# Kernel tuning notes

Measured on AMD Instinct MI355X. Metric: run time of the kernel, lower is better.

## Reference

```python
import jax, jax.numpy as jnp
import numpy as np

B, D, E, K, HID, RH, NL, EMB = 4096, 1024, 8, 2, 512, 256, 24, 32


def _ln(y, g, b, eps=1e-5):
    mu = y.mean(-1, keepdims=True)
    var = y.var(-1, keepdims=True)
    return (y - mu) / jnp.sqrt(var + eps) * g + b


def setup_inputs() -> dict:
    key = jax.random.key(0)
    ks = jax.random.split(key, 16)
    s = 0.02
    return {
        "h": jax.random.normal(ks[0], (B, D), jnp.float32),
        "x": jax.random.normal(ks[1], (B, D), jnp.float32),
        "layer_idx": 5,
        "layer_emb": jax.random.normal(ks[2], (NL, EMB)) * s,
        "phase_emb": jax.random.normal(ks[3], (2, EMB)) * s,
        "Wr1": jax.random.normal(ks[4], (2 * D + 2 * EMB, RH)) * s,
        "br1": jnp.zeros((RH,)),
        "lnr_g": jnp.ones((RH,)),
        "lnr_b": jnp.zeros((RH,)),
        "Wr2": jax.random.normal(ks[5], (RH, E)) * s,
        "br2": jnp.zeros((E,)),
        "W1": jax.random.normal(ks[6], (E, 2 * D, HID)) * s,
        "b1": jnp.zeros((E, HID)),
        "ln1_g": jnp.ones((E, HID)),
        "ln1_b": jnp.zeros((E, HID)),
        "W2": jax.random.normal(ks[7], (E, HID, 4 * D)) * s,
        "b2": jnp.zeros((E, 4 * D)),
        "Wa": jax.random.normal(ks[8], (E, D, D)) * s,
        "ba": jnp.zeros((E, D)),
        "Wb": jax.random.normal(ks[9], (E, D, D)) * s,
        "bb": jnp.zeros((E, D)),
        "Wg": jax.random.normal(ks[10], (E, D, D)) * s,
        "bg": jnp.zeros((E, D)),
        "Wv": jax.random.normal(ks[11], (E, D, D)) * s,
        "bv": jnp.zeros((E, D)),
    }


def reference(h, x, layer_idx, layer_emb, phase_emb, Wr1, br1, lnr_g, lnr_b,
              Wr2, br2, W1, b1, ln1_g, ln1_b, W2, b2,
              Wa, ba, Wb, bb, Wg, bg, Wv, bv):
    Bn = h.shape[0]
    # --- router ---
    le = jnp.broadcast_to(layer_emb[layer_idx], (Bn, EMB))
    pe = jnp.broadcast_to(phase_emb[0], (Bn, EMB))  # phase='equilibrium' -> idx 0
    ri = jnp.concatenate([h, x, le, pe], axis=-1)   # [B, 2D+64]
    rhid = jax.nn.gelu(_ln(ri @ Wr1 + br1, lnr_g, lnr_b), approximate=False)
    logits = rhid @ Wr2 + br2                       # [B, E]
    top_vals, top_idx = jax.lax.top_k(logits, K)    # [B, K]
    w = jax.nn.softmax(top_vals, axis=-1)           # [B, K]
    # --- all experts (vectorized over E), then gather top-k per token ---
    hx = jnp.concatenate([h, x], axis=-1)           # [B, 2D]
    hid = jnp.einsum('bi,eio->ebo', hx, W1) + b1[:, None]          # [E, B, HID]
    hid = jax.nn.gelu(_ln(hid, ln1_g[:, None], ln1_b[:, None]), approximate=False)
    feats = jnp.einsum('ebh,eho->ebo', hid, W2) + b2[:, None]      # [E, B, 4D]
    af, bf, gf, vf = jnp.split(feats, 4, axis=-1)
    alpha = jax.nn.sigmoid(jnp.einsum('ebd,edo->ebo', af, Wa) + ba[:, None])
    beta = jax.nn.softplus(jnp.einsum('ebd,edo->ebo', bf, Wb) + bb[:, None])
    gate = jax.nn.sigmoid(jnp.einsum('ebd,edo->ebo', gf, Wg) + bg[:, None])
    vcd = jnp.einsum('ebd,edo->ebo', vf, Wv) + bv[:, None]
    allo = jnp.stack([alpha, beta, gate, vcd])       # [4, E, B, D]
    sel = allo[:, top_idx, jnp.arange(Bn)[:, None]]  # [4, B, K, D]
    out = jnp.einsum('bk,obkd->obd', w, sel)         # [4, B, D]
    return out
```

## Files before the change

kernel.cpp:

```cpp
#include <hip/hip_runtime.h>
#include <hip/hip_bf16.h>

#define B_TOK   4096
#define D_DIM   1024
#define E_NUM   8
#define HID_DIM 512
#define RH_DIM  256
#define EMB_DIM 32
#define NPAIR   (B_TOK * 2)
#define CPAD    32

typedef __attribute__((ext_vector_type(8))) short    bf16x8;
typedef __attribute__((ext_vector_type(8))) unsigned short u16x8;
typedef __attribute__((ext_vector_type(4))) unsigned short u16x4;
typedef __attribute__((ext_vector_type(4))) float    f32x4;

__device__ __forceinline__ unsigned short f2bf(float f) {
    union { float f; unsigned u; } v; v.f = f;
    unsigned r = (v.u + 0x7fffu + ((v.u >> 16) & 1u)) >> 16;
    return (unsigned short)r;
}
__device__ __forceinline__ float bf2f(unsigned short b) {
    union { unsigned u; float f; } v; v.u = ((unsigned)b) << 16;
    return v.f;
}

__device__ __forceinline__ void glds16(const void* g, void* l) {
    __builtin_amdgcn_global_load_lds(
        (const __attribute__((address_space(1))) unsigned int*)g,
        (__attribute__((address_space(3))) unsigned int*)l, 16, 0, 0);
}

__device__ inline float apply_act(float v, int a) {
    if (a == 0 || a == 2) return 1.f / (1.f + __expf(-v));
    if (a == 1) return fmaxf(v, 0.f) + __logf(1.f + __expf(-fabsf(v)));
    return v;
}

__global__ void k_hxbf(const float* __restrict__ h, const float* __restrict__ x,
                       unsigned short* __restrict__ hi, unsigned short* __restrict__ lo) {
    int gid = blockIdx.x * 256 + threadIdx.x;
    int token = gid >> 8;
    int c0 = (gid & 255) * 8;
    const float* src = (c0 < 1024) ? (h + (size_t)token * 1024 + c0)
                                   : (x + (size_t)token * 1024 + c0 - 1024);
    u16x8 oh, ol;
#pragma unroll
    for (int j = 0; j < 8; ++j) {
        float f = src[j];
        unsigned short hb = f2bf(f);
        oh[j] = hb;
        ol[j] = f2bf(f - bf2f(hb));
    }
    size_t o = (size_t)gid * 8;
    *(u16x8*)(hi + o) = oh;
    *(u16x8*)(lo + o) = ol;
}

__global__ void k_cvtflat(const float* __restrict__ in, unsigned short* __restrict__ o8) {
    size_t gid = (size_t)blockIdx.x * 256 + threadIdx.x;
    const float4* s = (const float4*)(in + gid * 8);
    float4 a = s[0], b = s[1];
    u16x8 v;
    v[0] = f2bf(a.x); v[1] = f2bf(a.y); v[2] = f2bf(a.z); v[3] = f2bf(a.w);
    v[4] = f2bf(b.x); v[5] = f2bf(b.y); v[6] = f2bf(b.z); v[7] = f2bf(b.w);
    *(u16x8*)(o8 + gid * 8) = v;
}

template<bool SPLIT>
__global__ void k_convW(const float* __restrict__ in0, const float* __restrict__ in1,
                        const float* __restrict__ in2, const float* __restrict__ in3,
                        unsigned short* __restrict__ oh, unsigned short* __restrict__ ol,
                        int K, int N, int eper) {
    int z = blockIdx.z;
    int e = z % eper, m = z / eper;
    const float* in = (m == 0 ? in0 : m == 1 ? in1 : m == 2 ? in2 : in3) + (size_t)e * K * N;
    int n  = blockIdx.x * 256 + threadIdx.x;
    int kg = blockIdx.y;
    const float* ip = in + (size_t)kg * 8 * N + n;
    u16x8 hv, lv;
#pragma unroll
    for (int j = 0; j < 8; ++j) {
        float f = ip[(size_t)j * N];
        unsigned short hb = f2bf(f);
        hv[j] = hb;
        if (SPLIT) lv[j] = f2bf(f - bf2f(hb));
    }
    size_t o = (size_t)z * K * N + ((size_t)kg * N + n) * 8;
    *(u16x8*)(oh + o) = hv;
    if (SPLIT) *(u16x8*)(ol + o) = lv;
}

__global__ void k_bfuse(const float* __restrict__ b2,
                        const float* __restrict__ bo0, const float* __restrict__ bo1,
                        const float* __restrict__ bo2, const float* __restrict__ bo3,
                        const unsigned short* __restrict__ wsc,
                        float* __restrict__ bfused) {
    int zp = blockIdx.y; int e = zp & 7, o = zp >> 3;
    int col = blockIdx.x * 256 + threadIdx.x;
    __shared__ float b2s[1024];
    for (int i = threadIdx.x; i < 1024; i += 256)
        b2s[i] = b2[(size_t)e * 4096 + o * 1024 + i];
    __syncthreads();
    const unsigned short* W = wsc + (size_t)zp * 1024 * 1024;
    float acc = 0.f;
    for (int dg = 0; dg < 128; ++dg) {
        u16x8 w = *(const u16x8*)&W[((size_t)dg * 1024 + col) * 8];
#pragma unroll
        for (int j = 0; j < 8; ++j) acc += b2s[dg * 8 + j] * bf2f(w[j]);
    }
    const float* bo = (o == 0) ? bo0 : (o == 1) ? bo1 : (o == 2) ? bo2 : bo3;
    bfused[(size_t)e * 4096 + o * 1024 + col] = acc + bo[(size_t)e * 1024 + col];
}

__global__ void k_route(const float* __restrict__ Pf,
                        const int* __restrict__ lidx,
                        const float* __restrict__ layer_emb,
                        const float* __restrict__ phase_emb,
                        const float* __restrict__ Wr1, const float* __restrict__ br1,
                        const float* __restrict__ lnr_g, const float* __restrict__ lnr_b,
                        const float* __restrict__ Wr2, const float* __restrict__ br2,
                        float* __restrict__ pair_w,
                        int* __restrict__ lists, int* __restrict__ counts) {
    int b = blockIdx.x, t = threadIdx.x;
    __shared__ float sv[RH_DIM];
    __shared__ float a1[4], a2[4], mv[2];
    __shared__ float wsum[4][E_NUM];
    __shared__ float lg[E_NUM];
    __shared__ int sei[2];

    float rc = br1[t];
    {
        int li = lidx[0];
        for (int k = 0; k < EMB_DIM; ++k)
            rc += layer_emb[li * EMB_DIM + k] * Wr1[(2048 + k) * RH_DIM + t];
        for (int k = 0; k < EMB_DIM; ++k)
            rc += phase_emb[k] * Wr1[(2080 + k) * RH_DIM + t];
    }

    size_t idx = (size_t)b * RH_DIM + t;
    const size_t kstride = (size_t)B_TOK * RH_DIM;
    float y = ((Pf[idx] + Pf[idx + kstride]) + (Pf[idx + 2 * kstride] + Pf[idx + 3 * kstride]))
              + rc;
    float s1 = y, s2 = y * y;
    for (int o = 32; o; o >>= 1) { s1 += __shfl_down(s1, o); s2 += __shfl_down(s2, o); }
    if ((t & 63) == 0) { a1[t >> 6] = s1; a2[t >> 6] = s2; }
    __syncthreads();
    if (t == 0) {
        float S1 = a1[0] + a1[1] + a1[2] + a1[3];
        float S2 = a2[0] + a2[1] + a2[2] + a2[3];
        float mu = S1 / 256.f;
        mv[0] = mu;
        mv[1] = rsqrtf(S2 / 256.f - mu * mu + 1e-5f);
    }
    __syncthreads();
    float n = (y - mv[0]) * mv[1] * lnr_g[t] + lnr_b[t];
    sv[t] = 0.5f * n * (1.f + erff(n * 0.70710678118654752f));
    __syncthreads();

    {
        int e = t & 7, c = t >> 3;
        float part = 0.f;
#pragma unroll
        for (int jj = 0; jj < 8; ++jj)
            part += sv[c * 8 + jj] * Wr2[(c * 8 + jj) * E_NUM + e];
        part += __shfl_down(part, 8);
        part += __shfl_down(part, 16);
        part += __shfl_down(part, 32);
        if ((t & 63) < 8) wsum[t >> 6][e] = part;
    }
    __syncthreads();
    if (t < E_NUM)
        lg[t] = br2[t] + wsum[0][t] + wsum[1][t] + wsum[2][t] + wsum[3][t];
    __syncthreads();
    if (t == 0) {
        float v0 = -1e30f; int i0 = 0;
        for (int e = 0; e < E_NUM; ++e) if (lg[e] > v0) { v0 = lg[e]; i0 = e; }
        float v1 = -1e30f; int i1 = 0;
        for (int e = 0; e < E_NUM; ++e) if (e != i0 && lg[e] > v1) { v1 = lg[e]; i1 = e; }
        float e1 = expf(v1 - v0);
        pair_w[2 * b] = 1.f / (1.f + e1);
        pair_w[2 * b + 1] = e1 / (1.f + e1);
        sei[0] = i0; sei[1] = i1;
    }
    __syncthreads();
    if (t < 2) {
        int e = sei[t];
        int pos = atomicAdd(&counts[e * CPAD], 1);
        lists[e * B_TOK + pos] = 2 * b + t;
    }
}

__global__ void k_meta(const int* __restrict__ counts, const int* __restrict__ lists,
                       int* __restrict__ rowmap, int* __restrict__ row_e,
                       int* __restrict__ qof) {
    int q = blockIdx.x * 256 + threadIdx.x;
    int off_[E_NUM + 1]; off_[0] = 0;
#pragma unroll
    for (int i = 0; i < E_NUM; ++i) off_[i + 1] = off_[i] + counts[i * CPAD];
    int e = 0;
    while (e < E_NUM - 1 && q >= off_[e + 1]) ++e;
    int p = lists[e * B_TOK + (q - off_[e])];
    rowmap[q] = p;
    row_e[q] = e;
    qof[p] = q;
}

__global__ void k_lngelu(const float* __restrict__ hidp, const float* __restrict__ b1,
                         unsigned short* __restrict__ hidb, const int* __restrict__ row_e,
                         const float* __restrict__ g, const float* __restrict__ bb) {
    int q = blockIdx.x, t = threadIdx.x;
    int e = row_e[q];
    const size_t st = (size_t)NPAIR * HID_DIM;
    size_t o0 = (size_t)q * HID_DIM + t;
    float y0 = hidp[o0] + hidp[o0 + st] + b1[e * HID_DIM + t];
    float y1 = hidp[o0 + 256] + hidp[o0 + 256 + st] + b1[e * HID_DIM + t + 256];
    float s1 = y0 + y1, s2 = y0 * y0 + y1 * y1;
    for (int o = 32; o; o >>= 1) { s1 += __shfl_down(s1, o); s2 += __shfl_down(s2, o); }
    __shared__ float a1[4], a2[4], mv[2];
    if ((t & 63) == 0) { a1[t >> 6] = s1; a2[t >> 6] = s2; }
    __syncthreads();
    if (t == 0) {
        float S1 = a1[0] + a1[1] + a1[2] + a1[3];
        float S2 = a2[0] + a2[1] + a2[2] + a2[3];
        float mu = S1 / 512.f;
        mv[0] = mu;
        mv[1] = rsqrtf(S2 / 512.f - mu * mu + 1e-5f);
    }
    __syncthreads();
    const float* ge = g + e * HID_DIM;
    const float* be = bb + e * HID_DIM;
    float mu = mv[0], ir = mv[1];
    float n0 = (y0 - mu) * ir * ge[t] + be[t];
    float n1 = (y1 - mu) * ir * ge[t + 256] + be[t + 256];
    unsigned short* orow = hidb + (size_t)q * HID_DIM;
    orow[t]       = f2bf(0.5f * n0 * (1.f + erff(n0 * 0.70710678118654752f)));
    orow[t + 256] = f2bf(0.5f * n1 * (1.f + erff(n1 * 0.70710678118654752f)));
}

__global__ void k_comb(const unsigned short* __restrict__ sel,
                       const int* __restrict__ qof, const float* __restrict__ pw,
                       float* __restrict__ out) {
    int b = blockIdx.x, o = blockIdx.y;
    int c = threadIdx.x * 4;
    int q0 = qof[2 * b], q1 = qof[2 * b + 1];
    float w0 = pw[2 * b], w1 = pw[2 * b + 1];
    u16x4 a = __builtin_nontemporal_load((const u16x4*)(sel + (size_t)q0 * 4096 + o * 1024 + c));
    u16x4 bq = __builtin_nontemporal_load((const u16x4*)(sel + (size_t)q1 * 4096 + o * 1024 + c));
    f32x4 r;
#pragma unroll
    for (int j = 0; j < 4; ++j)
        r[j] = w0 * apply_act(bf2f(a[j]), o) + w1 * apply_act(bf2f(bq[j]), o);
    __builtin_nontemporal_store(r, (f32x4*)(out + ((size_t)o * B_TOK + b) * D_DIM + c));
}

template<int MODE, bool SPLIT, bool AGATHER, bool ZPIN>
__global__ __launch_bounds__(256)
void k_mm(const unsigned short* __restrict__ A, const unsigned short* __restrict__ Alo,
          int lda, int rowshift, int acol0,
          const unsigned short* __restrict__ Wp, const unsigned short* __restrict__ Wlo,
          size_t wstride,
          const float* __restrict__ bias, int bstride,
          float* __restrict__ Cf, unsigned short* __restrict__ Cb, int ldc,
          const int* __restrict__ counts, const int* __restrict__ rowmap, int Mfix,
          int N, int Kdim, int nz_e,
          float* __restrict__ outp, const float* __restrict__ pw) {
    const int gx = gridDim.x, gy = gridDim.y;
    unsigned fb = blockIdx.x + gx * (blockIdx.y + gy * blockIdx.z);
    int bx, byy, bz;
    if (ZPIN) {
        const unsigned nmn = gx * gy;
        unsigned xcd = fb & 7u, s = fb >> 3;
        bz  = xcd + 8u * (s / nmn);
        unsigned inner = s % nmn;
        bx  = inner % gx;
        byy = inner / gx;
    } else {
        unsigned xcd = fb & 7u, sb = fb >> 3;
        unsigned G = xcd + 8u * (sb / gx);
        bx  = sb % gx;
        byy = G % gy;
        bz  = G / gy;
    }

    const int e  = bz % nz_e;
    const int zq = bz / nz_e;
    int cnt = Mfix, base = 0;
    if (counts) {
        cnt = 0;
#pragma unroll
        for (int i = 0; i < E_NUM; ++i) {
            int c = counts[i * CPAD];
            if (i < e) base += c;
            if (i == e) cnt = c;
        }
    }
    const int m0 = byy * 128;
    if (m0 >= cnt) return;
    const int n0 = bx * 128;

    const size_t woff = (MODE == 8) ? (size_t)bz * wstride
                      : (MODE == 1 || MODE == 9) ? (size_t)e * wstride
                      : (size_t)e * wstride + (size_t)zq * Kdim * N;
    const unsigned short* W  = Wp + woff;
    const unsigned short* Wl = SPLIT ? (Wlo + woff) : nullptr;
    const float* bptr = (MODE == 1 || MODE == 9) ? bias + (size_t)e * bstride : nullptr;
    const int acol = acol0 + zq * Kdim;

    constexpr int ABUF = SPLIT ? 8192 : 4096;
    __shared__ unsigned short Alds[2][ABUF];
    __shared__ unsigned short Blds[2][ABUF];

    const int tid  = threadIdx.x;
    const int lane = tid & 63;
    const int wid  = tid >> 6;
    const int c0 = tid, c1 = tid + 256;
    const int r0 = c0 >> 2, r1 = c1 >> 2;

    auto aoff_of = [&](int r, int cq) -> size_t {
        int rr = m0 + r; if (rr >= cnt) rr = cnt - 1;
        int qg = base + rr;
        int row = AGATHER ? (rowmap[qg] >> rowshift)
                          : (MODE == 8 ? e * 512 + qg : qg);
        int slot = cq ^ ((r >> 1) & 3);
        return (size_t)row * lda + acol + (slot << 3);
    };
    size_t aoff0 = aoff_of(r0, c0 & 3);
    size_t aoff1 = aoff_of(r1, c1 & 3);
    const unsigned short* a0 = A + aoff0;
    const unsigned short* a1 = A + aoff1;
    const unsigned short* al0 = SPLIT ? Alo + aoff0 : nullptr;
    const unsigned short* al1 = SPLIT ? Alo + aoff1 : nullptr;
    size_t boff0 = ((size_t)(c0 >> 7) * N + n0 + (c0 & 127)) * 8;
    size_t boff1 = ((size_t)(c1 >> 7) * N + n0 + (c1 & 127)) * 8;
    const unsigned short* b0 = W + boff0;
    const unsigned short* b1 = W + boff1;
    const unsigned short* bl0 = SPLIT ? Wl + boff0 : nullptr;
    const unsigned short* bl1 = SPLIT ? Wl + boff1 : nullptr;

    const int d0 = c0 * 8, d1 = c1 * 8;
    const size_t bstep = (size_t)32 * N;

    auto stage = [&](int buf) {
        glds16(a0, &Alds[buf][d0]);
        glds16(a1, &Alds[buf][d1]);
        glds16(b0, &Blds[buf][d0]);
        glds16(b1, &Blds[buf][d1]);
        if constexpr (SPLIT) {
            glds16(al0, &Alds[buf][4096 + d0]);
            glds16(al1, &Alds[buf][4096 + d1]);
            glds16(bl0, &Blds[buf][4096 + d0]);
            glds16(bl1, &Blds[buf][4096 + d1]);
            al0 += 32; al1 += 32; bl0 += bstep; bl1 += bstep;
        }
        a0 += 32; a1 += 32; b0 += bstep; b1 += bstep;
    };

    const int wm = wid >> 1, wn = wid & 1;
    const int lr = lane & 15, lg = lane >> 4;
    const int aslot = (lg ^ ((lr >> 1) & 3)) << 3;

    f32x4 acc[4][4];
#pragma unroll
    for (int i = 0; i < 4; ++i)
#pragma unroll
        for (int j = 0; j < 4; ++j) acc[i][j] = (f32x4){0.f, 0.f, 0.f, 0.f};

    auto compute = [&](int b) {
        bf16x8 af[4], bfr[4];
#pragma unroll
        for (int i = 0; i < 4; ++i)
            af[i] = *(const bf16x8*)&Alds[b][(wm * 64 + i * 16 + lr) * 32 + aslot];
#pragma unroll
        for (int i = 0; i < 4; ++i)
            bfr[i] = *(const bf16x8*)&Blds[b][((lg << 7) + wn * 64 + i * 16 + lr) * 8];
        __builtin_amdgcn_s_setprio(1);
#pragma unroll
        for (int mi = 0; mi < 4; ++mi)
#pragma unroll
            for (int ni = 0; ni < 4; ++ni)
                acc[mi][ni] = __builtin_amdgcn_mfma_f32_16x16x32_bf16(af[mi], bfr[ni], acc[mi][ni], 0, 0, 0);
        if constexpr (SPLIT) {
            bf16x8 afl[4], bfl[4];
#pragma unroll
            for (int i = 0; i < 4; ++i)
                afl[i] = *(const bf16x8*)&Alds[b][4096 + (wm * 64 + i * 16 + lr) * 32 + aslot];
#pragma unroll
            for (int i = 0; i < 4; ++i)
                bfl[i] = *(const bf16x8*)&Blds[b][4096 + ((lg << 7) + wn * 64 + i * 16 + lr) * 8];
#pragma unroll
            for (int mi = 0; mi < 4; ++mi)
#pragma unroll
                for (int ni = 0; ni < 4; ++ni) {
                    acc[mi][ni] = __builtin_amdgcn_mfma_f32_16x16x32_bf16(af[mi],  bfl[ni], acc[mi][ni], 0, 0, 0);
                    acc[mi][ni] = __builtin_amdgcn_mfma_f32_16x16x32_bf16(afl[mi], bfr[ni], acc[mi][ni], 0, 0, 0);
                }
        }
        __builtin_amdgcn_s_setprio(0);
        __builtin_amdgcn_sched_barrier(0);
    };

    const int niter = Kdim / 32;
    stage(0);
    asm volatile("s_waitcnt vmcnt(0)" ::: "memory");
    __builtin_amdgcn_s_barrier();
    __builtin_amdgcn_sched_barrier(0);
    int cur = 0;
    for (int it = 0; it < niter; ++it) {
        const bool more = (it + 1 < niter);
        if (more) stage(cur ^ 1);
        compute(cur);
        if (more) {
            asm volatile("s_waitcnt vmcnt(0)" ::: "memory");
            __builtin_amdgcn_s_barrier();
            __builtin_amdgcn_sched_barrier(0);
        }
        cur ^= 1;
    }

    float bv[4];
#pragma unroll
    for (int ni = 0; ni < 4; ++ni)
        bv[ni] = (MODE == 1 || MODE == 9) ? bptr[n0 + wn * 64 + ni * 16 + lr] : 0.f;

#pragma unroll
    for (int mi = 0; mi < 4; ++mi) {
        int rbase = m0 + wm * 64 + mi * 16 + lg * 4;
#pragma unroll
        for (int rg = 0; rg < 4; ++rg) {
            int r = rbase + rg;
            if (r >= cnt) continue;
            int q = base + r;
#pragma unroll
            for (int ni = 0; ni < 4; ++ni) {
                int col = n0 + wn * 64 + ni * 16 + lr;
                float v = acc[mi][ni][rg] + bv[ni];
                if (MODE == 1) {
                    Cb[(size_t)q * ldc + col] = f2bf(v);
                } else if (MODE == 4) {
                    Cf[((size_t)zq * B_TOK + q) * ldc + col] = v;
                } else if (MODE == 5) {
                    Cf[((size_t)zq * NPAIR + q) * ldc + col] = v;
                } else if (MODE == 8) {
                    Cb[((size_t)e * 64 * 4096 + (size_t)(r >> 3) * 4096 + acol + col) * 8
                       + (r & 7)] = f2bf(v);
                } else {
                    int p = rowmap[q];
                    int o = col >> 10;
                    atomicAdd(outp + ((size_t)o * B_TOK + (p >> 1)) * D_DIM + (col & 1023),
                              pw[p] * apply_act(v, o));
                }
            }
        }
    }
}

extern "C" void kernel_launch(void* const* d_in, const int* in_sizes, int n_in,
                              void* d_out, int out_size, void* d_ws, size_t ws_size,
                              hipStream_t stream) {
    const float* h         = (const float*)d_in[0];
    const float* x         = (const float*)d_in[1];
    const int*   lidx      = (const int*)d_in[2];
    const float* layer_emb = (const float*)d_in[3];
    const float* phase_emb = (const float*)d_in[4];
    const float* Wr1       = (const float*)d_in[5];
    const float* br1       = (const float*)d_in[6];
    const float* lnr_g     = (const float*)d_in[7];
    const float* lnr_b     = (const float*)d_in[8];
    const float* Wr2       = (const float*)d_in[9];
    const float* br2       = (const float*)d_in[10];
    const float* W1        = (const float*)d_in[11];
    const float* b1        = (const float*)d_in[12];
    const float* ln1g      = (const float*)d_in[13];
    const float* ln1b      = (const float*)d_in[14];
    const float* W2        = (const float*)d_in[15];
    const float* b2        = (const float*)d_in[16];
    const float* Wa        = (const float*)d_in[17];
    const float* ba        = (const float*)d_in[18];
    const float* Wb_       = (const float*)d_in[19];
    const float* bbv       = (const float*)d_in[20];
    const float* Wg        = (const float*)d_in[21];
    const float* bg        = (const float*)d_in[22];
    const float* Wv        = (const float*)d_in[23];
    const float* bv        = (const float*)d_in[24];
    float* out = (float*)d_out;

    char* ws = (char*)d_ws;
    size_t off = 0;
    auto alloc = [&](size_t nb) { void* p = ws + off; off = (off + nb + 255) & ~(size_t)255; return p; };
    float*          pair_w  = (float*)alloc(NPAIR * 4);
    int*            counts  = (int*)alloc(E_NUM * CPAD * 4);
    int*            lists   = (int*)alloc((size_t)E_NUM * B_TOK * 4);
    int*            rowmap  = (int*)alloc(NPAIR * 4);
    int*            row_e   = (int*)alloc(NPAIR * 4);
    int*            qof     = (int*)alloc(NPAIR * 4);
    float*          bfused  = (float*)alloc((size_t)E_NUM * 4096 * 4);
    unsigned short* hx_hi   = (unsigned short*)alloc((size_t)B_TOK * 2048 * 2);
    unsigned short* hid_bf  = (unsigned short*)alloc((size_t)NPAIR * HID_DIM * 2);
    unsigned short* wsc_hi  = (unsigned short*)alloc((size_t)8 * 2048 * HID_DIM * 2);
    unsigned short* wsc_lo  = (unsigned short*)alloc((size_t)2048 * RH_DIM * 2);
    unsigned short* Wfused  = (unsigned short*)alloc((size_t)E_NUM * 64 * 4096 * 8 * 2);
    unsigned short* sel     = (unsigned short*)alloc((size_t)NPAIR * 4096 * 2);
    char*           scratch = (char*)alloc((size_t)34 << 20);
    const bool use_sel = (off <= ws_size);
    unsigned short* wsc4  = sel;
    unsigned short* W2bf  = (unsigned short*)scratch;
    unsigned short* hx_lo = (unsigned short*)scratch;
    float*          Pf    = (float*)(scratch + ((size_t)17 << 20));
    float*          hidp  = (float*)scratch;

    if (!use_sel) (void)hipMemsetAsync(d_out, 0, (size_t)out_size * 4, stream);
    (void)hipMemsetAsync(counts, 0, E_NUM * CPAD * 4, stream);

    k_hxbf<<<4096, 256, 0, stream>>>(h, x, hx_hi, hx_lo);
    k_convW<true><<<dim3(1, 256, 1), 256, 0, stream>>>(Wr1, nullptr, nullptr, nullptr,
                                                       wsc_hi, wsc_lo, 2048, RH_DIM, 1);
    k_mm<4, true, false, false><<<dim3(2, 32, 4), 256, 0, stream>>>(
        hx_hi, hx_lo, 2048, 0, 0, wsc_hi, wsc_lo, 0, nullptr, 0,
        Pf, nullptr, RH_DIM, nullptr, nullptr, B_TOK,
        RH_DIM, 512, 1, nullptr, nullptr);
    k_route<<<B_TOK, 256, 0, stream>>>(Pf, lidx, layer_emb, phase_emb, Wr1, br1,
                                       lnr_g, lnr_b, Wr2, br2,
                                       pair_w, lists, counts);
    k_meta<<<NPAIR / 256, 256, 0, stream>>>(counts, lists, rowmap, row_e, qof);

    k_convW<false><<<dim3(2, 256, 8), 256, 0, stream>>>(W1, nullptr, nullptr, nullptr,
                                                        wsc_hi, nullptr, 2048, HID_DIM, 8);
    k_mm<5, false, true, true><<<dim3(4, 32, 16), 256, 0, stream>>>(
        hx_hi, nullptr, 2048, 1, 0, wsc_hi, nullptr, (size_t)2048 * HID_DIM, nullptr, 0,
        hidp, nullptr, HID_DIM, counts, rowmap, 0,
        HID_DIM, 1024, 8, nullptr, nullptr);
    k_lngelu<<<NPAIR, 256, 0, stream>>>(hidp, b1, hid_bf, row_e, ln1g, ln1b);

    k_cvtflat<<<8192, 256, 0, stream>>>(W2, W2bf);
    k_convW<false><<<dim3(4, 128, 32), 256, 0, stream>>>(
        Wa, Wb_, Wg, Wv, wsc4, nullptr, D_DIM, D_DIM, 8);
    k_bfuse<<<dim3(4, 32), 256, 0, stream>>>(b2, ba, bbv, bg, bv, wsc4, bfused);
    k_mm<8, false, false, true><<<dim3(8, 4, 32), 256, 0, stream>>>(
        W2bf, nullptr, 4096, 0, 0,
        wsc4, nullptr, (size_t)D_DIM * D_DIM, nullptr, 0,
        nullptr, Wfused, 0, nullptr, nullptr, 512,
        D_DIM, D_DIM, 8, nullptr, nullptr);

    if (use_sel) {
        k_mm<1, false, false, true><<<dim3(32, 32, 8), 256, 0, stream>>>(
            hid_bf, nullptr, HID_DIM, 0, 0,
            Wfused, nullptr, (size_t)64 * 4096 * 8, bfused, 4096,
            nullptr, sel, 4096, counts, rowmap, 0,
            4096, HID_DIM, 8, nullptr, nullptr);
        k_comb<<<dim3(B_TOK, 4), 256, 0, stream>>>(sel, qof, pair_w, out);
    } else {
        k_mm<9, false, false, true><<<dim3(32, 32, 8), 256, 0, stream>>>(
            hid_bf, nullptr, HID_DIM, 0, 0,
            Wfused, nullptr, (size_t)64 * 4096 * 8, bfused, 4096,
            nullptr, nullptr, 0, counts, rowmap, 0,
            4096, HID_DIM, 8, out, pair_w);
    }
}
```

Measured before the change: 411.4 us.

## Make expert GEMMs persistent over M tiles and split N across z

The grouped expert GEMM kernel now loops over M tiles with a stride of gridDim.y instead of launching one block per possible tile and exiting early on empty ones. The per-expert grid height drops from 32 to 9, which cuts the number of idle blocks when expert token counts are uneven. For the main output GEMM, the N dimension is split into two halves carried on the z axis (a new Nfull stride plus a column offset), so more blocks are spread across experts. The cost is sequential tile processing inside a block and possible load imbalance when one expert receives many tokens.

```diff
diff --git a/kernel.cpp b/kernel.cpp
--- a/kernel.cpp
+++ b/kernel.cpp
@@ -263,7 +263,7 @@
           const float* __restrict__ bias, int bstride,
           float* __restrict__ Cf, unsigned short* __restrict__ Cb, int ldc,
           const int* __restrict__ counts, const int* __restrict__ rowmap, int Mfix,
-          int N, int Kdim, int nz_e,
+          int N, int Nfull, int Kdim, int nz_e,
           float* __restrict__ outp, const float* __restrict__ pw) {
     const int gx = gridDim.x, gy = gridDim.y;
     unsigned fb = blockIdx.x + gx * (blockIdx.y + gy * blockIdx.z);
@@ -295,8 +295,6 @@
             if (i == e) cnt = c;
         }
     }
-    const int m0 = byy * 128;
-    if (m0 >= cnt) return;
     const int n0 = bx * 128;
 
     const size_t woff = (MODE == 8) ? (size_t)bz * wstride
@@ -305,7 +303,8 @@
     const unsigned short* W  = Wp + woff;
     const unsigned short* Wl = SPLIT ? (Wlo + woff) : nullptr;
     const float* bptr = (MODE == 1 || MODE == 9) ? bias + (size_t)e * bstride : nullptr;
-    const int acol = acol0 + zq * Kdim;
+    const int acol = acol0 + ((MODE == 4 || MODE == 5 || MODE == 8) ? zq * Kdim : 0);
+    const int ncb  = (MODE == 1) ? zq * N : 0;
 
     constexpr int ABUF = SPLIT ? 8192 : 4096;
     __shared__ unsigned short Alds[2][ABUF];
@@ -317,138 +316,142 @@
     const int c0 = tid, c1 = tid + 256;
     const int r0 = c0 >> 2, r1 = c1 >> 2;
 
-    auto aoff_of = [&](int r, int cq) -> size_t {
-        int rr = m0 + r; if (rr >= cnt) rr = cnt - 1;
-        int qg = base + rr;
-        int row = AGATHER ? (rowmap[qg] >> rowshift)
-                          : (MODE == 8 ? e * 512 + qg : qg);
-        int slot = cq ^ ((r >> 1) & 3);
-        return (size_t)row * lda + acol + (slot << 3);
-    };
-    size_t aoff0 = aoff_of(r0, c0 & 3);
-    size_t aoff1 = aoff_of(r1, c1 & 3);
-    const unsigned short* a0 = A + aoff0;
-    const unsigned short* a1 = A + aoff1;
-    const unsigned short* al0 = SPLIT ? Alo + aoff0 : nullptr;
-    const unsigned short* al1 = SPLIT ? Alo + aoff1 : nullptr;
-    size_t boff0 = ((size_t)(c0 >> 7) * N + n0 + (c0 & 127)) * 8;
-    size_t boff1 = ((size_t)(c1 >> 7) * N + n0 + (c1 & 127)) * 8;
-    const unsigned short* b0 = W + boff0;
-    const unsigned short* b1 = W + boff1;
-    const unsigned short* bl0 = SPLIT ? Wl + boff0 : nullptr;
-    const unsigned short* bl1 = SPLIT ? Wl + boff1 : nullptr;
-
-    const int d0 = c0 * 8, d1 = c1 * 8;
-    const size_t bstep = (size_t)32 * N;
-
-    auto stage = [&](int buf) {
-        glds16(a0, &Alds[buf][d0]);
-        glds16(a1, &Alds[buf][d1]);
-        glds16(b0, &Blds[buf][d0]);
-        glds16(b1, &Blds[buf][d1]);
-        if constexpr (SPLIT) {
-            glds16(al0, &Alds[buf][4096 + d0]);
-            glds16(al1, &Alds[buf][4096 + d1]);
-            glds16(bl0, &Blds[buf][4096 + d0]);
-            glds16(bl1, &Blds[buf][4096 + d1]);
-            al0 += 32; al1 += 32; bl0 += bstep; bl1 += bstep;
-        }
-        a0 += 32; a1 += 32; b0 += bstep; b1 += bstep;
-    };
-
     const int wm = wid >> 1, wn = wid & 1;
     const int lr = lane & 15, lg = lane >> 4;
     const int aslot = (lg ^ ((lr >> 1) & 3)) << 3;
-
-    f32x4 acc[4][4];
-#pragma unroll
-    for (int i = 0; i < 4; ++i)
-#pragma unroll
-        for (int j = 0; j < 4; ++j) acc[i][j] = (f32x4){0.f, 0.f, 0.f, 0.f};
-
-    auto compute = [&](int b) {
-        bf16x8 af[4], bfr[4];
+    const int d0 = c0 * 8, d1 = c1 * 8;
+    const size_t bstep = (size_t)32 * Nfull;
+
+    for (int mt = byy; mt * 128 < cnt; mt += gy) {
+        const int m0 = mt * 128;
+
+        auto aoff_of = [&](int r, int cq) -> size_t {
+            int rr = m0 + r; if (rr >= cnt) rr = cnt - 1;
+            int qg = base + rr;
+            int row = AGATHER ? (rowmap[qg] >> rowshift)
+                              : (MODE == 8 ? e * 512 + qg : qg);
+            int slot = cq ^ ((r >> 1) & 3);
+            return (size_t)row * lda + acol + (slot << 3);
+        };
+        size_t aoff0 = aoff_of(r0, c0 & 3);
+        size_t aoff1 = aoff_of(r1, c1 & 3);
+        const unsigned short* a0 = A + aoff0;
+        const unsigned short* a1 = A + aoff1;
+        const unsigned short* al0 = SPLIT ? Alo + aoff0 : nullptr;
+        const unsigned short* al1 = SPLIT ? Alo + aoff1 : nullptr;
+        size_t boff0 = ((size_t)(c0 >> 7) * Nfull + ncb + n0 + (c0 & 127)) * 8;
+        size_t boff1 = ((size_t)(c1 >> 7) * Nfull + ncb + n0 + (c1 & 127)) * 8;
+        const unsigned short* b0 = W + boff0;
+        const unsigned short* b1 = W + boff1;
+        const unsigned short* bl0 = SPLIT ? Wl + boff0 : nullptr;
+        const unsigned short* bl1 = SPLIT ? Wl + boff1 : nullptr;
+
+        auto stage = [&](int buf) {
+            glds16(a0, &Alds[buf][d0]);
+            glds16(a1, &Alds[buf][d1]);
+            glds16(b0, &Blds[buf][d0]);
+            glds16(b1, &Blds[buf][d1]);
+            if constexpr (SPLIT) {
+                glds16(al0, &Alds[buf][4096 + d0]);
+                glds16(al1, &Alds[buf][4096 + d1]);
+                glds16(bl0, &Blds[buf][4096 + d0]);
+                glds16(bl1, &Blds[buf][4096 + d1]);
+                al0 += 32; al1 += 32; bl0 += bstep; bl1 += bstep;
+            }
+            a0 += 32; a1 += 32; b0 += bstep; b1 += bstep;
+        };
+
+        f32x4 acc[4][4];
 #pragma unroll
         for (int i = 0; i < 4; ++i)
-            af[i] = *(const bf16x8*)&Alds[b][(wm * 64 + i * 16 + lr) * 32 + aslot];
-#pragma unroll
-        for (int i = 0; i < 4; ++i)
-            bfr[i] = *(const bf16x8*)&Blds[b][((lg << 7) + wn * 64 + i * 16 + lr) * 8];
-        __builtin_amdgcn_s_setprio(1);
-#pragma unroll
-        for (int mi = 0; mi < 4; ++mi)
-#pragma unroll
-            for (int ni = 0; ni < 4; ++ni)
-                acc[mi][ni] = __builtin_amdgcn_mfma_f32_16x16x32_bf16(af[mi], bfr[ni], acc[mi][ni], 0, 0, 0);
-        if constexpr (SPLIT) {
-            bf16x8 afl[4], bfl[4];
+#pragma unroll
+            for (int j = 0; j < 4; ++j) acc[i][j] = (f32x4){0.f, 0.f, 0.f, 0.f};
+
+        auto compute = [&](int b) {
+            bf16x8 af[4], bfr[4];
 #pragma unroll
             for (int i = 0; i < 4; ++i)
-                afl[i] = *(const bf16x8*)&Alds[b][4096 + (wm * 64 + i * 16 + lr) * 32 + aslot];
+                af[i] = *(const bf16x8*)&Alds[b][(wm * 64 + i * 16 + lr) * 32 + aslot];
 #pragma unroll
             for (int i = 0; i < 4; ++i)
-                bfl[i] = *(const bf16x8*)&Blds[b][4096 + ((lg << 7) + wn * 64 + i * 16 + lr) * 8];
+                bfr[i] = *(const bf16x8*)&Blds[b][((lg << 7) + wn * 64 + i * 16 + lr) * 8];
+            __builtin_amdgcn_s_setprio(1);
 #pragma unroll
             for (int mi = 0; mi < 4; ++mi)
 #pragma unroll
+                for (int ni = 0; ni < 4; ++ni)
+                    acc[mi][ni] = __builtin_amdgcn_mfma_f32_16x16x32_bf16(af[mi], bfr[ni], acc[mi][ni], 0, 0, 0);
+            if constexpr (SPLIT) {
+                bf16x8 afl[4], bfl[4];
+#pragma unroll
+                for (int i = 0; i < 4; ++i)
+                    afl[i] = *(const bf16x8*)&Alds[b][4096 + (wm * 64 + i * 16 + lr) * 32 + aslot];
+#pragma unroll
+                for (int i = 0; i < 4; ++i)
+                    bfl[i] = *(const bf16x8*)&Blds[b][4096 + ((lg << 7) + wn * 64 + i * 16 + lr) * 8];
+#pragma unroll
+                for (int mi = 0; mi < 4; ++mi)
+#pragma unroll
+                    for (int ni = 0; ni < 4; ++ni) {
+                        acc[mi][ni] = __builtin_amdgcn_mfma_f32_16x16x32_bf16(af[mi],  bfl[ni], acc[mi][ni], 0, 0, 0);
+                        acc[mi][ni] = __builtin_amdgcn_mfma_f32_16x16x32_bf16(afl[mi], bfr[ni], acc[mi][ni], 0, 0, 0);
+                    }
+            }
+            __builtin_amdgcn_s_setprio(0);
+            __builtin_amdgcn_sched_barrier(0);
+        };
+
+        const int niter = Kdim / 32;
+        stage(0);
+        asm volatile("s_waitcnt vmcnt(0)" ::: "memory");
+        __builtin_amdgcn_s_barrier();
+        __builtin_amdgcn_sched_barrier(0);
+        int cur = 0;
+        for (int it = 0; it < niter; ++it) {
+            const bool more = (it + 1 < niter);
+            if (more) stage(cur ^ 1);
+            compute(cur);
+            if (more) {
+                asm volatile("s_waitcnt vmcnt(0)" ::: "memory");
+                __builtin_amdgcn_s_barrier();
+                __builtin_amdgcn_sched_barrier(0);
+            }
+            cur ^= 1;
+        }
+        __builtin_amdgcn_s_barrier();
+
+        float bv[4];
+#pragma unroll
+        for (int ni = 0; ni < 4; ++ni)
+            bv[ni] = (MODE == 1 || MODE == 9) ? bptr[ncb + n0 + wn * 64 + ni * 16 + lr] : 0.f;
+
+#pragma unroll
+        for (int mi = 0; mi < 4; ++mi) {
+            int rbase = m0 + wm * 64 + mi * 16 + lg * 4;
+#pragma unroll
+            for (int rg = 0; rg < 4; ++rg) {
+                int r = rbase + rg;
+                if (r >= cnt) continue;
+                int q = base + r;
+#pragma unroll
                 for (int ni = 0; ni < 4; ++ni) {
-                    acc[mi][ni] = __builtin_amdgcn_mfma_f32_16x16x32_bf16(af[mi],  bfl[ni], acc[mi][ni], 0, 0, 0);
-                    acc[mi][ni] = __builtin_amdgcn_mfma_f32_16x16x32_bf16(afl[mi], bfr[ni], acc[mi][ni], 0, 0, 0);
-                }
-        }
-        __builtin_amdgcn_s_setprio(0);
-        __builtin_amdgcn_sched_barrier(0);
-    };
-
-    const int niter = Kdim / 32;
-    stage(0);
-    asm volatile("s_waitcnt vmcnt(0)" ::: "memory");
-    __builtin_amdgcn_s_barrier();
-    __builtin_amdgcn_sched_barrier(0);
-    int cur = 0;
-    for (int it = 0; it < niter; ++it) {
-        const bool more = (it + 1 < niter);
-        if (more) stage(cur ^ 1);
-        compute(cur);
-        if (more) {
-            asm volatile("s_waitcnt vmcnt(0)" ::: "memory");
-            __builtin_amdgcn_s_barrier();
-            __builtin_amdgcn_sched_barrier(0);
-        }
-        cur ^= 1;
-    }
-
-    float bv[4];
-#pragma unroll
-    for (int ni = 0; ni < 4; ++ni)
-        bv[ni] = (MODE == 1 || MODE == 9) ? bptr[n0 + wn * 64 + ni * 16 + lr] : 0.f;
-
-#pragma unroll
-    for (int mi = 0; mi < 4; ++mi) {
-        int rbase = m0 + wm * 64 + mi * 16 + lg * 4;
-#pragma unroll
-        for (int rg = 0; rg < 4; ++rg) {
-            int r = rbase + rg;
-            if (r >= cnt) continue;
-            int q = base + r;
-#pragma unroll
-            for (int ni = 0; ni < 4; ++ni) {
-                int col = n0 + wn * 64 + ni * 16 + lr;
-                float v = acc[mi][ni][rg] + bv[ni];
-                if (MODE == 1) {
-                    Cb[(size_t)q * ldc + col] = f2bf(v);
-                } else if (MODE == 4) {
-                    Cf[((size_t)zq * B_TOK + q) * ldc + col] = v;
-                } else if (MODE == 5) {
-                    Cf[((size_t)zq * NPAIR + q) * ldc + col] = v;
-                } else if (MODE == 8) {
-                    Cb[((size_t)e * 64 * 4096 + (size_t)(r >> 3) * 4096 + acol + col) * 8
-                       + (r & 7)] = f2bf(v);
-                } else {
-                    int p = rowmap[q];
-                    int o = col >> 10;
-                    atomicAdd(outp + ((size_t)o * B_TOK + (p >> 1)) * D_DIM + (col & 1023),
-                              pw[p] * apply_act(v, o));
+                    int col = ncb + n0 + wn * 64 + ni * 16 + lr;
+                    float v = acc[mi][ni][rg] + bv[ni];
+                    if (MODE == 1) {
+                        Cb[(size_t)q * ldc + col] = f2bf(v);
+                    } else if (MODE == 4) {
+                        Cf[((size_t)zq * B_TOK + q) * ldc + col] = v;
+                    } else if (MODE == 5) {
+                        Cf[((size_t)zq * NPAIR + q) * ldc + col] = v;
+                    } else if (MODE == 8) {
+                        Cb[((size_t)e * 64 * 4096 + (size_t)(r >> 3) * 4096 + acol + col) * 8
+                           + (r & 7)] = f2bf(v);
+                    } else {
+                        int p = rowmap[q];
+                        int o = col >> 10;
+                        atomicAdd(outp + ((size_t)o * B_TOK + (p >> 1)) * D_DIM + (col & 1023),
+                                  pw[p] * apply_act(v, o));
+                    }
                 }
             }
         }
@@ -518,7 +521,7 @@
     k_mm<4, true, false, false><<<dim3(2, 32, 4), 256, 0, stream>>>(
         hx_hi, hx_lo, 2048, 0, 0, wsc_hi, wsc_lo, 0, nullptr, 0,
         Pf, nullptr, RH_DIM, nullptr, nullptr, B_TOK,
-        RH_DIM, 512, 1, nullptr, nullptr);
+        RH_DIM, RH_DIM, 512, 1, nullptr, nullptr);
     k_route<<<B_TOK, 256, 0, stream>>>(Pf, lidx, layer_emb, phase_emb, Wr1, br1,
                                        lnr_g, lnr_b, Wr2, br2,
                                        pair_w, lists, counts);
@@ -526,10 +529,10 @@
 
     k_convW<false><<<dim3(2, 256, 8), 256, 0, stream>>>(W1, nullptr, nullptr, nullptr,
                                                         wsc_hi, nullptr, 2048, HID_DIM, 8);
-    k_mm<5, false, true, true><<<dim3(4, 32, 16), 256, 0, stream>>>(
+    k_mm<5, false, true, true><<<dim3(4, 9, 16), 256, 0, stream>>>(
         hx_hi, nullptr, 2048, 1, 0, wsc_hi, nullptr, (size_t)2048 * HID_DIM, nullptr, 0,
         hidp, nullptr, HID_DIM, counts, rowmap, 0,
-        HID_DIM, 1024, 8, nullptr, nullptr);
+        HID_DIM, HID_DIM, 1024, 8, nullptr, nullptr);
     k_lngelu<<<NPAIR, 256, 0, stream>>>(hidp, b1, hid_bf, row_e, ln1g, ln1b);
 
     k_cvtflat<<<8192, 256, 0, stream>>>(W2, W2bf);
@@ -540,20 +543,20 @@
         W2bf, nullptr, 4096, 0, 0,
         wsc4, nullptr, (size_t)D_DIM * D_DIM, nullptr, 0,
         nullptr, Wfused, 0, nullptr, nullptr, 512,
-        D_DIM, D_DIM, 8, nullptr, nullptr);
+        D_DIM, D_DIM, D_DIM, 8, nullptr, nullptr);
 
     if (use_sel) {
-        k_mm<1, false, false, true><<<dim3(32, 32, 8), 256, 0, stream>>>(
+        k_mm<1, false, false, true><<<dim3(16, 9, 16), 256, 0, stream>>>(
             hid_bf, nullptr, HID_DIM, 0, 0,
             Wfused, nullptr, (size_t)64 * 4096 * 8, bfused, 4096,
             nullptr, sel, 4096, counts, rowmap, 0,
-            4096, HID_DIM, 8, nullptr, nullptr);
+            2048, 4096, HID_DIM, 8, nullptr, nullptr);
         k_comb<<<dim3(B_TOK, 4), 256, 0, stream>>>(sel, qof, pair_w, out);
     } else {
         k_mm<9, false, false, true><<<dim3(32, 32, 8), 256, 0, stream>>>(
             hid_bf, nullptr, HID_DIM, 0, 0,
             Wfused, nullptr, (size_t)64 * 4096 * 8, bfused, 4096,
             nullptr, nullptr, 0, counts, rowmap, 0,
-            4096, HID_DIM, 8, out, pair_w);
-    }
-}
+            4096, 4096, HID_DIM, 8, out, pair_w);
+    }
+}
```

Measured after the change: 422.4 us. +2.7%, slower.
